# Optimization experiments

Hardware: AMD Instinct MI355X
Metric: run time of the kernel (lower is better)

Reference implementation:

```python
import jax, jax.numpy as jnp
import numpy as np

# Structural constants (init_kwargs)
NUM_IN = 4096        # input nodes
L = 8                # hidden topological levels
H = 32768            # hidden units per level
K = 32               # fan-in per hidden unit
O = 256              # output nodes
KO = 64              # fan-in per output unit
SCALE = 4.9          # config.SCALE_ACTIVATION (NEAT default)
B = 128              # batch (original is 1; vmapped for scale)
EXTRAS = L * H + O   # non-input nodes, initialized to ones like the original


def setup_inputs() -> dict:
    key = jax.random.key(0)
    kx, kidx, kwh, kwo = jax.random.split(key, 4)
    x = jax.random.normal(kx, (B, NUM_IN), jnp.float32)
    # Level-l units may only read nodes already computed: index < NUM_IN + l*H
    idx_levels = [
        jax.random.randint(jax.random.fold_in(kidx, l), (H, K), 0, NUM_IN + l * H, dtype=jnp.int32)
        for l in range(L)
    ]
    idx_hidden = jnp.stack(idx_levels)  # [L, H, K]
    w_hidden = jax.random.normal(kwh, (L, H, K), jnp.float32) * 0.1
    idx_out = jax.random.randint(jax.random.fold_in(kidx, L), (O, KO), 0, NUM_IN + L * H, dtype=jnp.int32)
    w_out = jax.random.normal(kwo, (O, KO), jnp.float32) * 0.1
    return {"x": x, "w_hidden": w_hidden, "w_out": w_out,
            "idx_hidden": idx_hidden, "idx_out": idx_out}


def reference(x, w_hidden, w_out, idx_hidden, idx_out):
    # Faithful to FeedForwardNet.forward: buffer = cat(inputs, ones(extras));
    # per node: gather -> 1-output linear (no bias) -> scale -> sigmoid -> scatter.
    def single(xi):  # xi: [NUM_IN]
        buf = jnp.concatenate([xi, jnp.ones((EXTRAS,), xi.dtype)])  # [NUM_IN+EXTRAS]
        for l in range(L):  # fixed topological levels (small, structural loop)
            gathered = buf[idx_hidden[l]]                              # [H, K]
            pre = SCALE * jnp.einsum('hk,hk->h', gathered, w_hidden[l])
            buf = buf.at[NUM_IN + l * H: NUM_IN + (l + 1) * H].set(jax.nn.sigmoid(pre))
        go = buf[idx_out]                                              # [O, KO]
        return jax.nn.sigmoid(SCALE * jnp.einsum('ok,ok->o', go, w_out))
    return jax.vmap(single)(x)  # [B, O]
```

## Files before the change

kernel.cpp:

```cpp
#include <hip/hip_runtime.h>

#define BATCH   128
#define NUM_IN  4096
#define LVL     8
#define HID     32768
#define KH      32
#define OUTN    256
#define KOUT    64
#define SCALEA  4.9f

#define QR      6.0f
#define QSTEP   (2.0f * QR / 255.0f)
#define INV255  (1.0f / 255.0f)


__device__ __forceinline__ unsigned short f2bf(float f) {
    unsigned u = __float_as_uint(f);
    u += 0x7FFFu + ((u >> 16) & 1u);
    return (unsigned short)(u >> 16);
}
__device__ __forceinline__ float bf_lo(unsigned u) { return __uint_as_float(u << 16); }
__device__ __forceinline__ float bf_hi(unsigned u) { return __uint_as_float(u & 0xFFFF0000u); }

__device__ __forceinline__ unsigned q_in(float x) {
    float t = (x + QR) * (255.0f / (2.0f * QR));
    t = fminf(fmaxf(t, 0.f), 255.f);
    return __float2uint_rn(t);
}

__global__ __launch_bounds__(256) void transpose_x(const float* __restrict__ x,
                                                   unsigned* __restrict__ in_bf,
                                                   unsigned short* __restrict__ ext) {
    __shared__ float lds[64][129];
    const int n0 = blockIdx.x * 64;
    const int t  = threadIdx.x;
    #pragma unroll
    for (int it = 0; it < 32; ++it) {
        int i = it * 256 + t;
        int b = i >> 6;
        int n = i & 63;
        lds[n][b] = x[b * NUM_IN + n0 + n];
    }
    __syncthreads();
    #pragma unroll
    for (int it = 0; it < 16; ++it) {
        int i  = it * 256 + t;
        int n  = i >> 6;
        int bp = i & 63;
        float v0 = lds[n][2 * bp], v1 = lds[n][2 * bp + 1];
        in_bf[(n0 + n) * 64 + bp] = (unsigned)f2bf(v0) | ((unsigned)f2bf(v1) << 16);
        ext[(unsigned)(n0 + n) * 64 + bp] =
            (unsigned short)(q_in(v0) | (q_in(v1) << 8));
    }
}

__global__ __launch_bounds__(256) void level0(const unsigned* __restrict__ in_bf,
                                              unsigned short* __restrict__ ext,
                                              const int* __restrict__ idx,
                                              const float* __restrict__ w) {
    const int lane = threadIdx.x & 63;
    int h = (blockIdx.x << 2) + (threadIdx.x >> 6);
    h = __builtin_amdgcn_readfirstlane(h);
    const int*   ip = idx + h * KH;
    const float* wp = w   + h * KH;
    float ax = 0.f, ay = 0.f;
    #pragma unroll
    for (int k = 0; k < KH; ++k) {
        int   j  = __builtin_amdgcn_readfirstlane(ip[k]);
        float wk = wp[k];
        unsigned v = in_bf[(unsigned)j * 64 + lane];
        ax = fmaf(wk, bf_lo(v), ax);
        ay = fmaf(wk, bf_hi(v), ay);
    }
    unsigned qx = __float2uint_rn(255.f / (1.f + __expf(-SCALEA * ax)));
    unsigned qy = __float2uint_rn(255.f / (1.f + __expf(-SCALEA * ay)));
    ext[(unsigned)(NUM_IN + h) * 64 + lane] = (unsigned short)(qx | (qy << 8));
}

__global__ __launch_bounds__(256) void deep_level(unsigned short* __restrict__ ext,
                                                  const int* __restrict__ idx,
                                                  const float* __restrict__ w,
                                                  int nbase) {
    const int lane = threadIdx.x & 63;
    int h = (blockIdx.x << 2) + (threadIdx.x >> 6);
    h = __builtin_amdgcn_readfirstlane(h);
    const int*   ip = idx + h * KH;
    const float* wp = w   + h * KH;

    float ax = 0.f, ay = 0.f, bias = 0.f;
    #pragma unroll
    for (int k = 0; k < KH; ++k) {
        int   j  = __builtin_amdgcn_readfirstlane(ip[k]);
        float wk = wp[k];
        bool isin = (j < NUM_IN);
        float a = wk * (isin ? QSTEP : INV255);
        bias   += isin ? (-QR * wk) : 0.f;
        unsigned t = ext[(unsigned)j * 64 + lane];
        ax = fmaf(a, (float)(t & 0xFFu), ax);
        ay = fmaf(a, (float)(t >> 8),   ay);
    }
    ax += bias;
    ay += bias;

    unsigned qx = __float2uint_rn(255.f / (1.f + __expf(-SCALEA * ax)));
    unsigned qy = __float2uint_rn(255.f / (1.f + __expf(-SCALEA * ay)));
    ext[(unsigned)(nbase + h) * 64 + lane] = (unsigned short)(qx | (qy << 8));
}

__global__ __launch_bounds__(256) void output_layer(const unsigned short* __restrict__ ext,
                                                    const int* __restrict__ idx,
                                                    const float* __restrict__ w,
                                                    float* __restrict__ out) {
    const int lane = threadIdx.x & 63;
    int o = (blockIdx.x << 2) + (threadIdx.x >> 6);
    o = __builtin_amdgcn_readfirstlane(o);
    const int*   ip = idx + o * KOUT;
    const float* wp = w   + o * KOUT;

    float ax = 0.f, ay = 0.f, bias = 0.f;
    #pragma unroll
    for (int k = 0; k < KOUT; ++k) {
        int   j  = __builtin_amdgcn_readfirstlane(ip[k]);
        float wk = wp[k];
        bool isin = (j < NUM_IN);
        float a = wk * (isin ? QSTEP : INV255);
        bias   += isin ? (-QR * wk) : 0.f;
        unsigned t = ext[(unsigned)j * 64 + lane];
        ax = fmaf(a, (float)(t & 0xFFu), ax);
        ay = fmaf(a, (float)(t >> 8),   ay);
    }
    ax += bias;
    ay += bias;
    out[(2 * lane + 0) * OUTN + o] = 1.f / (1.f + __expf(-SCALEA * ax));
    out[(2 * lane + 1) * OUTN + o] = 1.f / (1.f + __expf(-SCALEA * ay));
}

extern "C" void kernel_launch(void* const* d_in, const int* in_sizes, int n_in,
                              void* d_out, int out_size, void* d_ws, size_t ws_size,
                              hipStream_t stream) {
    const float* x          = (const float*)d_in[0];
    const float* w_hidden   = (const float*)d_in[1];
    const float* w_out      = (const float*)d_in[2];
    const int*   idx_hidden = (const int*)  d_in[3];
    const int*   idx_out    = (const int*)  d_in[4];
    float* out = (float*)d_out;

    char* ws = (char*)d_ws;
    unsigned*       in_bf = (unsigned*)      (ws + 0);
    unsigned short* ext   = (unsigned short*)(ws + 1048576);

    transpose_x<<<NUM_IN / 64, 256, 0, stream>>>(x, in_bf, ext);

    level0<<<HID / 4, 256, 0, stream>>>(in_bf, ext, idx_hidden, w_hidden);
    for (int l = 1; l < LVL; ++l) {
        deep_level<<<HID / 4, 256, 0, stream>>>(
            ext,
            idx_hidden + (size_t)l * HID * KH,
            w_hidden   + (size_t)l * HID * KH,
            NUM_IN + l * HID);
    }
    output_layer<<<OUTN / 4, 256, 0, stream>>>(ext, idx_out, w_out, out);
}
```

Before: 264.9 us.

## Shard activation buffer by batch slice to shrink per-gather footprint

Reorganizes the quantized activation buffer into 8 batch shards, each holding 8 packed batch pairs (16 bytes) per node, instead of 128 bytes per node. Each wavefront now processes 8 nodes with 8 lanes each, and blocks are interleaved across shards so that shards sharing a node index can hit in cache together. The aim is to raise gather efficiency and cache locality, since each shard's working set is smaller. The cost is that indices and weights become per-lane vector loads instead of scalar broadcasts, and each idx/w element is now read by 8 blocks instead of one.

```diff
diff --git a/kernel.cpp b/kernel.cpp
--- a/kernel.cpp
+++ b/kernel.cpp
@@ -12,6 +12,8 @@
 #define QR      6.0f
 #define QSTEP   (2.0f * QR / 255.0f)
 #define INV255  (1.0f / 255.0f)
+#define NT      (NUM_IN + LVL * HID)
+#define NSH     8
 
 
 __device__ __forceinline__ unsigned short f2bf(float f) {
@@ -49,7 +51,7 @@
         int bp = i & 63;
         float v0 = lds[n][2 * bp], v1 = lds[n][2 * bp + 1];
         in_bf[(n0 + n) * 64 + bp] = (unsigned)f2bf(v0) | ((unsigned)f2bf(v1) << 16);
-        ext[(unsigned)(n0 + n) * 64 + bp] =
+        ext[((size_t)(bp >> 3) * NT + (n0 + n)) * 8 + (bp & 7)] =
             (unsigned short)(q_in(v0) | (q_in(v1) << 8));
     }
 }
@@ -74,28 +76,31 @@
     }
     unsigned qx = __float2uint_rn(255.f / (1.f + __expf(-SCALEA * ax)));
     unsigned qy = __float2uint_rn(255.f / (1.f + __expf(-SCALEA * ay)));
-    ext[(unsigned)(NUM_IN + h) * 64 + lane] = (unsigned short)(qx | (qy << 8));
+    ext[((size_t)(lane >> 3) * NT + (NUM_IN + h)) * 8 + (lane & 7)] =
+        (unsigned short)(qx | (qy << 8));
 }
 
 __global__ __launch_bounds__(256) void deep_level(unsigned short* __restrict__ ext,
                                                   const int* __restrict__ idx,
                                                   const float* __restrict__ w,
                                                   int nbase) {
+    const int s    = blockIdx.x & 7;
     const int lane = threadIdx.x & 63;
-    int h = (blockIdx.x << 2) + (threadIdx.x >> 6);
-    h = __builtin_amdgcn_readfirstlane(h);
+    const int g    = lane >> 3, r = lane & 7;
+    const int h    = (blockIdx.x >> 3) * 32 + (threadIdx.x >> 6) * 8 + g;
+    unsigned short* sh = ext + (size_t)s * NT * 8;
     const int*   ip = idx + h * KH;
     const float* wp = w   + h * KH;
 
     float ax = 0.f, ay = 0.f, bias = 0.f;
     #pragma unroll
     for (int k = 0; k < KH; ++k) {
-        int   j  = __builtin_amdgcn_readfirstlane(ip[k]);
+        int   j  = ip[k];
         float wk = wp[k];
+        unsigned t = sh[(unsigned)j * 8 + r];
         bool isin = (j < NUM_IN);
         float a = wk * (isin ? QSTEP : INV255);
-        bias   += isin ? (-QR * wk) : 0.f;
-        unsigned t = ext[(unsigned)j * 64 + lane];
+        bias += isin ? (-QR * wk) : 0.f;
         ax = fmaf(a, (float)(t & 0xFFu), ax);
         ay = fmaf(a, (float)(t >> 8),   ay);
     }
@@ -104,35 +109,38 @@
 
     unsigned qx = __float2uint_rn(255.f / (1.f + __expf(-SCALEA * ax)));
     unsigned qy = __float2uint_rn(255.f / (1.f + __expf(-SCALEA * ay)));
-    ext[(unsigned)(nbase + h) * 64 + lane] = (unsigned short)(qx | (qy << 8));
+    sh[(unsigned)(nbase + h) * 8 + r] = (unsigned short)(qx | (qy << 8));
 }
 
 __global__ __launch_bounds__(256) void output_layer(const unsigned short* __restrict__ ext,
                                                     const int* __restrict__ idx,
                                                     const float* __restrict__ w,
                                                     float* __restrict__ out) {
+    const int s    = blockIdx.x & 7;
     const int lane = threadIdx.x & 63;
-    int o = (blockIdx.x << 2) + (threadIdx.x >> 6);
-    o = __builtin_amdgcn_readfirstlane(o);
+    const int g    = lane >> 3, r = lane & 7;
+    const int o    = (blockIdx.x >> 3) * 32 + (threadIdx.x >> 6) * 8 + g;
+    const unsigned short* sh = ext + (size_t)s * NT * 8;
     const int*   ip = idx + o * KOUT;
     const float* wp = w   + o * KOUT;
 
     float ax = 0.f, ay = 0.f, bias = 0.f;
     #pragma unroll
     for (int k = 0; k < KOUT; ++k) {
-        int   j  = __builtin_amdgcn_readfirstlane(ip[k]);
+        int   j  = ip[k];
         float wk = wp[k];
+        unsigned t = sh[(unsigned)j * 8 + r];
         bool isin = (j < NUM_IN);
         float a = wk * (isin ? QSTEP : INV255);
-        bias   += isin ? (-QR * wk) : 0.f;
-        unsigned t = ext[(unsigned)j * 64 + lane];
+        bias += isin ? (-QR * wk) : 0.f;
         ax = fmaf(a, (float)(t & 0xFFu), ax);
         ay = fmaf(a, (float)(t >> 8),   ay);
     }
     ax += bias;
     ay += bias;
-    out[(2 * lane + 0) * OUTN + o] = 1.f / (1.f + __expf(-SCALEA * ax));
-    out[(2 * lane + 1) * OUTN + o] = 1.f / (1.f + __expf(-SCALEA * ay));
+    int b0 = s * 16 + 2 * r;
+    out[(b0 + 0) * OUTN + o] = 1.f / (1.f + __expf(-SCALEA * ax));
+    out[(b0 + 1) * OUTN + o] = 1.f / (1.f + __expf(-SCALEA * ay));
 }
 
 extern "C" void kernel_launch(void* const* d_in, const int* in_sizes, int n_in,
@@ -153,11 +161,11 @@
 
     level0<<<HID / 4, 256, 0, stream>>>(in_bf, ext, idx_hidden, w_hidden);
     for (int l = 1; l < LVL; ++l) {
-        deep_level<<<HID / 4, 256, 0, stream>>>(
+        deep_level<<<(HID / 32) * NSH, 256, 0, stream>>>(
             ext,
             idx_hidden + (size_t)l * HID * KH,
             w_hidden   + (size_t)l * HID * KH,
             NUM_IN + l * HID);
     }
-    output_layer<<<OUTN / 4, 256, 0, stream>>>(ext, idx_out, w_out, out);
+    output_layer<<<(OUTN / 32) * NSH, 256, 0, stream>>>(ext, idx_out, w_out, out);
 }
```

After: 466.4 us. +76.1%, slower.
